# Kernel optimization log

Hardware: AMD Instinct MI355X
Metric: run time of the kernel (lower is better)

## Reference

```python
import jax, jax.numpy as jnp
import numpy as np

B, S, D = 16, 577, 768
H = 12
DH = D // H  # 64


def setup_inputs() -> dict:
    key = jax.random.key(0)
    ks = jax.random.split(key, 7)
    s = 0.02
    return {
        "hidden_states": jax.random.normal(ks[0], (B, S, D), dtype=jnp.float32),
        "wq": jax.random.normal(ks[1], (D, D), dtype=jnp.float32) * s,
        "bq": jnp.zeros((D,), dtype=jnp.float32),
        "wk": jax.random.normal(ks[2], (D, D), dtype=jnp.float32) * s,
        "bk": jnp.zeros((D,), dtype=jnp.float32),
        "wv": jax.random.normal(ks[3], (D, D), dtype=jnp.float32) * s,
        "bv": jnp.zeros((D,), dtype=jnp.float32),
    }


def reference(hidden_states, wq, bq, wk, bk, wv, bv):
    # Linear projections (torch nn.Linear: x @ W^T + b)
    q = hidden_states @ wq.T + bq  # [B,S,D]
    k = hidden_states @ wk.T + bk
    v = hidden_states @ wv.T + bv

    def split_heads(x):
        return x.reshape(B, S, H, DH).transpose(0, 2, 1, 3)  # [B,H,S,DH]

    q, k, v = split_heads(q), split_heads(k), split_heads(v)
    scale = 1.0 / jnp.sqrt(jnp.float32(DH))
    scores = jnp.einsum("bhqd,bhkd->bhqk", q, k) * scale  # [B,H,S,S]
    probs = jax.nn.softmax(scores, axis=-1)
    ctx = jnp.einsum("bhqk,bhkd->bhqd", probs, v)  # [B,H,S,DH]
    ctx = ctx.transpose(0, 2, 1, 3).reshape(B, S, D)
    return ctx, probs
```

## Files before the change

kernel.cpp:

```cpp
#include <hip/hip_runtime.h>
#include <hip/hip_bf16.h>
#include <cstdint>

#define B_  16
#define S_  577
#define D_  768
#define H_  12
#define SP  640
#define M_  (B_*S_)
#define MP  9344
#define N_  2304
#define SCS 664

typedef __attribute__((ext_vector_type(8))) short short8;
typedef __attribute__((ext_vector_type(4))) float f32x4;

static __device__ __forceinline__ unsigned short f2bf(float f) {
    uint32_t u = __builtin_bit_cast(uint32_t, f);
    uint32_t r = u + 0x7fffu + ((u >> 16) & 1u);
    return (unsigned short)(r >> 16);
}
static __device__ __forceinline__ float bf2f(unsigned short u) {
    uint32_t x = ((uint32_t)u) << 16;
    return __builtin_bit_cast(float, x);
}

typedef unsigned int u32;
typedef __attribute__((address_space(3))) u32 lds_u32;
typedef __attribute__((address_space(1))) const u32 gbl_u32;
static __device__ __forceinline__ void gll16(const void* g, void* l) {
    __builtin_amdgcn_global_load_lds((gbl_u32*)g, (lds_u32*)l, 16, 0, 0);
}


__global__ __launch_bounds__(256) void prep(
    const float* __restrict__ X,
    const float* __restrict__ Wq, const float* __restrict__ Wk, const float* __restrict__ Wv,
    unsigned short* __restrict__ Xb, unsigned short* __restrict__ Wb)
{
    const int NT1 = MP * 192;
    const int NT2 = N_ * 192;
    const int total = NT1 + NT2;
    const int stride = gridDim.x * 256;
    for (int i = blockIdx.x * 256 + threadIdx.x; i < total; i += stride) {
        if (i < NT1) {
            int row = i / 192, c4 = i - row * 192;
            uint2 out = make_uint2(0u, 0u);
            if (row < M_) {
                float4 v = *(const float4*)(X + (size_t)row * 768 + c4 * 4);
                unsigned short p[4] = { f2bf(v.x), f2bf(v.y), f2bf(v.z), f2bf(v.w) };
                out = *(uint2*)p;
            }
            *(uint2*)(Xb + (size_t)row * 768 + c4 * 4) = out;
        } else {
            int j = i - NT1;
            int row = j / 192, c4 = j - row * 192;
            const float* src = (row < 768) ? (Wq + (size_t)row * 768)
                             : (row < 1536) ? (Wk + (size_t)(row - 768) * 768)
                                            : (Wv + (size_t)(row - 1536) * 768);
            float4 v = *(const float4*)(src + c4 * 4);
            unsigned short p[4] = { f2bf(v.x), f2bf(v.y), f2bf(v.z), f2bf(v.w) };
            *(uint2*)(Wb + (size_t)row * 768 + c4 * 4) = *(uint2*)p;
        }
    }
}

__global__ __launch_bounds__(256) void qkv_gemm(
    const unsigned short* __restrict__ Xb, const unsigned short* __restrict__ Wb,
    const float* __restrict__ bq, const float* __restrict__ bk, const float* __restrict__ bv,
    unsigned short* __restrict__ Qf, unsigned short* __restrict__ Kf,
    unsigned short* __restrict__ Vf)
{
    __shared__ unsigned short Als[128 * 64];
    __shared__ unsigned short Bls[128 * 64];

    const int mt = blockIdx.x, nt = blockIdx.y;
    const int tid = threadIdx.x, lane = tid & 63, wid = tid >> 6;
    const int wm = wid >> 1, wn = wid & 1;
    const int m0 = mt * 128, n0 = nt * 128;
    const int prow = lane >> 3;
    const int pc8  = lane & 7;

    f32x4 acc[4][4] = {};

    for (int kk = 0; kk < 768; kk += 64) {
        __syncthreads();
        #pragma unroll
        for (int t = 0; t < 4; ++t) {
            int row  = wid * 32 + t * 8 + prow;
            int scol = ((pc8 ^ (row & 7)) * 8);
            gll16(Xb + (size_t)(m0 + row) * 768 + kk + scol, &Als[(wid * 32 + t * 8) * 64]);
            gll16(Wb + (size_t)(n0 + row) * 768 + kk + scol, &Bls[(wid * 32 + t * 8) * 64]);
        }
        __syncthreads();

        #pragma unroll
        for (int ks = 0; ks < 2; ++ks) {
            short8 af[4], bfv[4];
            #pragma unroll
            for (int i = 0; i < 4; ++i) {
                int row = wm * 64 + i * 16 + (lane & 15);
                af[i] = *(const short8*)&Als[row * 64 + (((ks * 4 + (lane >> 4)) ^ (row & 7)) * 8)];
            }
            #pragma unroll
            for (int j = 0; j < 4; ++j) {
                int row = wn * 64 + j * 16 + (lane & 15);
                bfv[j] = *(const short8*)&Bls[row * 64 + (((ks * 4 + (lane >> 4)) ^ (row & 7)) * 8)];
            }
            #pragma unroll
            for (int i = 0; i < 4; ++i)
                #pragma unroll
                for (int j = 0; j < 4; ++j)
                    acc[i][j] = __builtin_amdgcn_mfma_f32_16x16x32_bf16(af[i], bfv[j], acc[i][j], 0, 0, 0);
        }
    }

    #pragma unroll
    for (int j = 0; j < 4; ++j) {
        int n = n0 + wn * 64 + j * 16 + (lane & 15);
        float bias = (n < 768) ? bq[n] : (n < 1536) ? bk[n - 768] : bv[n - 1536];
        int nn  = (n < 768) ? n : (n < 1536) ? n - 768 : n - 1536;
        int hh  = nn >> 6, dwh = nn & 63;
        #pragma unroll
        for (int i = 0; i < 4; ++i) {
            #pragma unroll
            for (int r = 0; r < 4; ++r) {
                int m = m0 + wm * 64 + i * 16 + (lane >> 4) * 4 + r;
                if (m >= M_) continue;
                int b = m / 577;
                int s = m - b * 577;
                float val = acc[i][j][r] + bias;
                size_t bh = (size_t)b * 12 + hh;
                if (n < 768) {
                    size_t off = (((size_t)(b * 40 + (s >> 4)) * 12 + hh) * 2 + (dwh >> 5)) * 512
                               + (s & 15) * 32 + ((dwh >> 3) & 3) * 8 + (dwh & 7);
                    Qf[off] = f2bf(val * 0.125f);
                } else if (n < 1536) {
                    size_t off = ((bh * 10 + (s >> 6)) * 8 + ((s >> 4) & 3) * 2 + (dwh >> 5)) * 512
                               + (s & 15) * 32 + ((dwh >> 3) & 3) * 8 + (dwh & 7);
                    Kf[off] = f2bf(val);
                } else {
                    size_t off = ((bh * 20 + (s >> 5)) * 4 + (dwh >> 4)) * 512
                               + (dwh & 15) * 32 + ((s >> 3) & 3) * 8 + (s & 7);
                    Vf[off] = f2bf(val);
                }
            }
        }
    }
}

__global__ __launch_bounds__(256) void attn(
    const unsigned short* __restrict__ Qf, const unsigned short* __restrict__ Kf,
    const unsigned short* __restrict__ Vf,
    float* __restrict__ ctx, float* __restrict__ probs)
{
    __shared__ unsigned short sc[16 * SCS];
    __shared__ float rowinv[16];

    const int wg  = blockIdx.x;
    const int idx = (wg & 7) * 888 + (wg >> 3);
    const int bh  = idx / 37;
    const int qt  = idx - bh * 37;
    const int h   = bh % 12, b = bh / 12;

    const int tid = threadIdx.x, lane = tid & 63, wid = tid >> 6;
    const int l15 = lane & 15, g = lane >> 4;
    const int q0 = qt * 16;
    const int lofs = l15 * 32 + g * 8;

    const unsigned short* qb = Qf + ((size_t)(b * 40 + qt) * 12 + h) * 1024 + lofs;
    short8 aq0 = *(const short8*)qb;
    short8 aq1 = *(const short8*)(qb + 512);

    const unsigned short* kb0 = Kf + (size_t)bh * 40960 + wid * 1024 + lofs;
    #pragma unroll
    for (int c = 0; c < 10; ++c) {
        const unsigned short* kb = kb0 + c * 4096;
        short8 bk0 = *(const short8*)kb;
        short8 bk1 = *(const short8*)(kb + 512);
        f32x4 s4 = {};
        s4 = __builtin_amdgcn_mfma_f32_16x16x32_bf16(aq0, bk0, s4, 0, 0, 0);
        s4 = __builtin_amdgcn_mfma_f32_16x16x32_bf16(aq1, bk1, s4, 0, 0, 0);
        int key = c * 64 + wid * 16 + l15;
        #pragma unroll
        for (int r = 0; r < 4; ++r)
            sc[(g * 4 + r) * SCS + key] = (key < S_) ? f2bf(s4[r]) : (unsigned short)0xFF80u;
    }
    __syncthreads();

    const int r = tid >> 4, c0 = tid & 15;
    unsigned short* row = &sc[r * SCS];
    float m = -1e30f;
    #pragma unroll
    for (int i = 0; i < 5; ++i) {
        short8 v = *(const short8*)&row[(c0 + 16 * i) * 8];
        #pragma unroll
        for (int jj = 0; jj < 8; ++jj) m = fmaxf(m, bf2f((unsigned short)v[jj]));
    }
    #pragma unroll
    for (int o = 8; o; o >>= 1) m = fmaxf(m, __shfl_xor(m, o));

    float ssum = 0.f;
    #pragma unroll
    for (int i = 0; i < 5; ++i) {
        short8 v = *(const short8*)&row[(c0 + 16 * i) * 8];
        short8 w;
        #pragma unroll
        for (int jj = 0; jj < 8; ++jj) {
            float e = __expf(bf2f((unsigned short)v[jj]) - m);
            ssum += e;
            w[jj] = (short)f2bf(e);
        }
        *(short8*)&row[(c0 + 16 * i) * 8] = w;
    }
    #pragma unroll
    for (int o = 8; o; o >>= 1) ssum += __shfl_xor(ssum, o);
    float inv = 1.0f / ssum;
    if (c0 == 0) rowinv[r] = inv;
    __syncthreads();

    int q = q0 + r;
    if (q < S_) {
        float* prow = probs + ((size_t)bh * S_ + q) * S_;
        #pragma unroll
        for (int i = 0; i < 5; ++i) {
            int ch = c0 + 16 * i;
            short8 v = *(const short8*)&row[ch * 8];
            if (ch < 72) {
                float4 o0, o1;
                o0.x = bf2f((unsigned short)v[0]) * inv; o0.y = bf2f((unsigned short)v[1]) * inv;
                o0.z = bf2f((unsigned short)v[2]) * inv; o0.w = bf2f((unsigned short)v[3]) * inv;
                o1.x = bf2f((unsigned short)v[4]) * inv; o1.y = bf2f((unsigned short)v[5]) * inv;
                o1.z = bf2f((unsigned short)v[6]) * inv; o1.w = bf2f((unsigned short)v[7]) * inv;
                *(float4*)&prow[ch * 8]     = o0;
                *(float4*)&prow[ch * 8 + 4] = o1;
            } else if (ch == 72) {
                prow[576] = bf2f((unsigned short)v[0]) * inv;
            }
        }
    }

    f32x4 oc = {};
    const unsigned short* vb0 = Vf + (size_t)bh * 40960 + wid * 512 + lofs;
    const unsigned short* pb  = &sc[l15 * SCS + g * 8];
    #pragma unroll
    for (int kk = 0; kk < 20; ++kk) {
        short8 ap = *(const short8*)(pb + kk * 32);
        short8 bv = *(const short8*)(vb0 + kk * 2048);
        oc = __builtin_amdgcn_mfma_f32_16x16x32_bf16(ap, bv, oc, 0, 0, 0);
    }
    #pragma unroll
    for (int rr = 0; rr < 4; ++rr) {
        int qr = g * 4 + rr;
        int qq = q0 + qr;
        if (qq < S_)
            ctx[((size_t)b * S_ + qq) * D_ + h * 64 + wid * 16 + l15] = oc[rr] * rowinv[qr];
    }
}

extern "C" void kernel_launch(void* const* d_in, const int* in_sizes, int n_in,
                              void* d_out, int out_size, void* d_ws, size_t ws_size,
                              hipStream_t stream) {
    const float* X  = (const float*)d_in[0];
    const float* Wq = (const float*)d_in[1];
    const float* bq = (const float*)d_in[2];
    const float* Wk = (const float*)d_in[3];
    const float* bk = (const float*)d_in[4];
    const float* Wv = (const float*)d_in[5];
    const float* bv = (const float*)d_in[6];

    float* ctx   = (float*)d_out;
    float* probs = ctx + (size_t)B_ * S_ * D_;

    unsigned short* Xb = (unsigned short*)probs;
    unsigned short* Wb = Xb + (size_t)MP * 768;

    unsigned short* Qf = (unsigned short*)d_ws;
    unsigned short* Kf = Qf + (size_t)7864320;
    unsigned short* Vf = Kf + (size_t)7864320;

    prep<<<dim3(1024), 256, 0, stream>>>(X, Wq, Wk, Wv, Xb, Wb);
    qkv_gemm<<<dim3(73, 18), 256, 0, stream>>>(Xb, Wb, bq, bk, bv, Qf, Kf, Vf);
    attn<<<dim3(7104), 256, 0, stream>>>(Qf, Kf, Vf, ctx, probs);
}
```

Baseline: 215.3 us.

## Vectorize Q/K epilogue stores via operand swap, fold log2e, nontemporal outputs

For the Q and K column tiles the GEMM swaps the MFMA operands so each lane holds four consecutive head-dim values, which lets it write packed 8-byte stores instead of scalar 2-byte scattered stores. The log2(e)/sqrt(d) factor is folded into the Q scale so softmax can use exp2f. Probs and ctx are written with nontemporal stores to reduce cache pollution from the large output. The prep kernel now also zeroes the V padding keys 577..639, which guards the padded region that attention reads.

```diff
diff --git a/kernel.cpp b/kernel.cpp
--- a/kernel.cpp
+++ b/kernel.cpp
@@ -11,6 +11,7 @@
 #define MP  9344
 #define N_  2304
 #define SCS 664
+#define QSCALE 0.18033688011112042f
 
 typedef __attribute__((ext_vector_type(8))) short short8;
 typedef __attribute__((ext_vector_type(4))) float f32x4;
@@ -36,11 +37,13 @@
 __global__ __launch_bounds__(256) void prep(
     const float* __restrict__ X,
     const float* __restrict__ Wq, const float* __restrict__ Wk, const float* __restrict__ Wv,
-    unsigned short* __restrict__ Xb, unsigned short* __restrict__ Wb)
+    unsigned short* __restrict__ Xb, unsigned short* __restrict__ Wb,
+    unsigned short* __restrict__ Vf)
 {
     const int NT1 = MP * 192;
     const int NT2 = N_ * 192;
-    const int total = NT1 + NT2;
+    const int VPAD = 192 * 64 * 63;
+    const int total = NT1 + NT2 + VPAD;
     const int stride = gridDim.x * 256;
     for (int i = blockIdx.x * 256 + threadIdx.x; i < total; i += stride) {
         if (i < NT1) {
@@ -52,7 +55,7 @@
                 out = *(uint2*)p;
             }
             *(uint2*)(Xb + (size_t)row * 768 + c4 * 4) = out;
-        } else {
+        } else if (i < NT1 + NT2) {
             int j = i - NT1;
             int row = j / 192, c4 = j - row * 192;
             const float* src = (row < 768) ? (Wq + (size_t)row * 768)
@@ -61,6 +64,13 @@
             float4 v = *(const float4*)(src + c4 * 4);
             unsigned short p[4] = { f2bf(v.x), f2bf(v.y), f2bf(v.z), f2bf(v.w) };
             *(uint2*)(Wb + (size_t)row * 768 + c4 * 4) = *(uint2*)p;
+        } else {
+            int j = i - NT1 - NT2;
+            int bh = j / (64 * 63), rem = j - bh * (64 * 63);
+            int d = rem / 63, key = 577 + (rem - d * 63);
+            size_t off = (((size_t)bh * 20 + (key >> 5)) * 4 + (d >> 4)) * 512
+                       + (d & 15) * 32 + ((key >> 3) & 3) * 8 + (key & 7);
+            Vf[off] = 0;
         }
     }
 }
@@ -75,11 +85,15 @@
     __shared__ unsigned short Bls[128 * 64];
 
     const int mt = blockIdx.x, nt = blockIdx.y;
+    const bool qk = (nt < 12);
     const int tid = threadIdx.x, lane = tid & 63, wid = tid >> 6;
     const int wm = wid >> 1, wn = wid & 1;
     const int m0 = mt * 128, n0 = nt * 128;
-    const int prow = lane >> 3;
-    const int pc8  = lane & 7;
+    const int l15 = lane & 15, g = lane >> 4;
+    const int prow = lane >> 3, pc8 = lane & 7;
+
+    const unsigned short* Pa = qk ? Bls : Als;
+    const unsigned short* Pb = qk ? Als : Bls;
 
     f32x4 acc[4][4] = {};
 
@@ -96,51 +110,72 @@
 
         #pragma unroll
         for (int ks = 0; ks < 2; ++ks) {
-            short8 af[4], bfv[4];
+            short8 fa[4], fb[4];
             #pragma unroll
             for (int i = 0; i < 4; ++i) {
-                int row = wm * 64 + i * 16 + (lane & 15);
-                af[i] = *(const short8*)&Als[row * 64 + (((ks * 4 + (lane >> 4)) ^ (row & 7)) * 8)];
+                int row = wm * 64 + i * 16 + l15;
+                fa[i] = *(const short8*)&Pa[row * 64 + (((ks * 4 + g) ^ (row & 7)) * 8)];
             }
             #pragma unroll
             for (int j = 0; j < 4; ++j) {
-                int row = wn * 64 + j * 16 + (lane & 15);
-                bfv[j] = *(const short8*)&Bls[row * 64 + (((ks * 4 + (lane >> 4)) ^ (row & 7)) * 8)];
+                int row = wn * 64 + j * 16 + l15;
+                fb[j] = *(const short8*)&Pb[row * 64 + (((ks * 4 + g) ^ (row & 7)) * 8)];
             }
             #pragma unroll
             for (int i = 0; i < 4; ++i)
                 #pragma unroll
                 for (int j = 0; j < 4; ++j)
-                    acc[i][j] = __builtin_amdgcn_mfma_f32_16x16x32_bf16(af[i], bfv[j], acc[i][j], 0, 0, 0);
-        }
-    }
-
-    #pragma unroll
-    for (int j = 0; j < 4; ++j) {
-        int n = n0 + wn * 64 + j * 16 + (lane & 15);
-        float bias = (n < 768) ? bq[n] : (n < 1536) ? bk[n - 768] : bv[n - 1536];
-        int nn  = (n < 768) ? n : (n < 1536) ? n - 768 : n - 1536;
-        int hh  = nn >> 6, dwh = nn & 63;
+                    acc[i][j] = __builtin_amdgcn_mfma_f32_16x16x32_bf16(fa[i], fb[j], acc[i][j], 0, 0, 0);
+        }
+    }
+
+    if (qk) {
+        const float* bb = (nt < 6) ? bq : bk;
+        unsigned short* Dst = (nt < 6) ? Qf : Kf;
+        const float scale = (nt < 6) ? QSCALE : 1.0f;
         #pragma unroll
         for (int i = 0; i < 4; ++i) {
-            #pragma unroll
-            for (int r = 0; r < 4; ++r) {
-                int m = m0 + wm * 64 + i * 16 + (lane >> 4) * 4 + r;
+            int nrow0 = n0 - ((nt < 6) ? 0 : 768) + wm * 64 + i * 16 + g * 4;
+            float4 b4 = *(const float4*)(bb + nrow0);
+            int hh = nrow0 >> 6, d0 = nrow0 & 63;
+            int dh5 = d0 >> 5;
+            int dsub = ((d0 >> 3) & 3) * 8 + (d0 & 7);
+            #pragma unroll
+            for (int j = 0; j < 4; ++j) {
+                int m = m0 + wn * 64 + j * 16 + l15;
                 if (m >= M_) continue;
-                int b = m / 577;
-                int s = m - b * 577;
-                float val = acc[i][j][r] + bias;
-                size_t bh = (size_t)b * 12 + hh;
-                if (n < 768) {
-                    size_t off = (((size_t)(b * 40 + (s >> 4)) * 12 + hh) * 2 + (dwh >> 5)) * 512
-                               + (s & 15) * 32 + ((dwh >> 3) & 3) * 8 + (dwh & 7);
-                    Qf[off] = f2bf(val * 0.125f);
-                } else if (n < 1536) {
-                    size_t off = ((bh * 10 + (s >> 6)) * 8 + ((s >> 4) & 3) * 2 + (dwh >> 5)) * 512
-                               + (s & 15) * 32 + ((dwh >> 3) & 3) * 8 + (dwh & 7);
-                    Kf[off] = f2bf(val);
-                } else {
-                    size_t off = ((bh * 20 + (s >> 5)) * 4 + (dwh >> 4)) * 512
+                int b = m / 577, s = m - b * 577;
+                unsigned short p[4];
+                p[0] = f2bf((acc[i][j][0] + b4.x) * scale);
+                p[1] = f2bf((acc[i][j][1] + b4.y) * scale);
+                p[2] = f2bf((acc[i][j][2] + b4.z) * scale);
+                p[3] = f2bf((acc[i][j][3] + b4.w) * scale);
+                size_t off;
+                if (nt < 6)
+                    off = (((size_t)(b * 40 + (s >> 4)) * 12 + hh) * 2 + dh5) * 512
+                        + (s & 15) * 32 + dsub;
+                else
+                    off = ((((size_t)(b * 12 + hh)) * 10 + (s >> 6)) * 8 + ((s >> 4) & 3) * 2 + dh5) * 512
+                        + (s & 15) * 32 + dsub;
+                *(uint2*)(Dst + off) = *(uint2*)p;
+            }
+        }
+    } else {
+        #pragma unroll
+        for (int j = 0; j < 4; ++j) {
+            int n = n0 + wn * 64 + j * 16 + l15;
+            int nn = n - 1536;
+            float bias = bv[nn];
+            int hh = nn >> 6, dwh = nn & 63;
+            #pragma unroll
+            for (int i = 0; i < 4; ++i) {
+                #pragma unroll
+                for (int r = 0; r < 4; ++r) {
+                    int m = m0 + wm * 64 + i * 16 + g * 4 + r;
+                    if (m >= M_) continue;
+                    int b = m / 577, s = m - b * 577;
+                    float val = acc[i][j][r] + bias;
+                    size_t off = (((size_t)(b * 12 + hh) * 20 + (s >> 5)) * 4 + (dwh >> 4)) * 512
                                + (dwh & 15) * 32 + ((s >> 3) & 3) * 8 + (s & 7);
                     Vf[off] = f2bf(val);
                 }
@@ -207,7 +242,7 @@
         short8 w;
         #pragma unroll
         for (int jj = 0; jj < 8; ++jj) {
-            float e = __expf(bf2f((unsigned short)v[jj]) - m);
+            float e = exp2f(bf2f((unsigned short)v[jj]) - m);
             ssum += e;
             w[jj] = (short)f2bf(e);
         }
@@ -227,15 +262,15 @@
             int ch = c0 + 16 * i;
             short8 v = *(const short8*)&row[ch * 8];
             if (ch < 72) {
-                float4 o0, o1;
-                o0.x = bf2f((unsigned short)v[0]) * inv; o0.y = bf2f((unsigned short)v[1]) * inv;
-                o0.z = bf2f((unsigned short)v[2]) * inv; o0.w = bf2f((unsigned short)v[3]) * inv;
-                o1.x = bf2f((unsigned short)v[4]) * inv; o1.y = bf2f((unsigned short)v[5]) * inv;
-                o1.z = bf2f((unsigned short)v[6]) * inv; o1.w = bf2f((unsigned short)v[7]) * inv;
-                *(float4*)&prow[ch * 8]     = o0;
-                *(float4*)&prow[ch * 8 + 4] = o1;
+                f32x4 o0, o1;
+                o0[0] = bf2f((unsigned short)v[0]) * inv; o0[1] = bf2f((unsigned short)v[1]) * inv;
+                o0[2] = bf2f((unsigned short)v[2]) * inv; o0[3] = bf2f((unsigned short)v[3]) * inv;
+                o1[0] = bf2f((unsigned short)v[4]) * inv; o1[1] = bf2f((unsigned short)v[5]) * inv;
+                o1[2] = bf2f((unsigned short)v[6]) * inv; o1[3] = bf2f((unsigned short)v[7]) * inv;
+                __builtin_nontemporal_store(o0, (f32x4*)&prow[ch * 8]);
+                __builtin_nontemporal_store(o1, (f32x4*)&prow[ch * 8 + 4]);
             } else if (ch == 72) {
-                prow[576] = bf2f((unsigned short)v[0]) * inv;
+                __builtin_nontemporal_store(bf2f((unsigned short)v[0]) * inv, &prow[576]);
             }
         }
     }
@@ -254,7 +289,8 @@
         int qr = g * 4 + rr;
         int qq = q0 + qr;
         if (qq < S_)
-            ctx[((size_t)b * S_ + qq) * D_ + h * 64 + wid * 16 + l15] = oc[rr] * rowinv[qr];
+            __builtin_nontemporal_store(oc[rr] * rowinv[qr],
+                &ctx[((size_t)b * S_ + qq) * D_ + h * 64 + wid * 16 + l15]);
     }
 }
 
@@ -279,7 +315,7 @@
     unsigned short* Kf = Qf + (size_t)7864320;
     unsigned short* Vf = Kf + (size_t)7864320;
 
-    prep<<<dim3(1024), 256, 0, stream>>>(X, Wq, Wk, Wv, Xb, Wb);
+    prep<<<dim3(1024), 256, 0, stream>>>(X, Wq, Wk, Wv, Xb, Wb, Vf);
     qkv_gemm<<<dim3(73, 18), 256, 0, stream>>>(Xb, Wb, bq, bk, bv, Qf, Kf, Vf);
     attn<<<dim3(7104), 256, 0, stream>>>(Qf, Kf, Vf, ctx, probs);
 }
```

Result: no change. 213.0 us (-1.1%).
